# Performance work log

Measured on AMD Instinct MI355X. Metric: run time of the kernel, lower is better.

## Reference

```python
import jax, jax.numpy as jnp
import numpy as np

N = 16384      # total nodes (hits)
K = 8          # n_neighbors
NB = 8         # number of graphs in batch
IN_C = 6       # in_channels
HID = 128      # hidden_channels
NCLS = 3       # num_classes
SLOPE = 0.2    # GATv2 leaky_relu negative_slope
BIG = 1e30     # mask value for cross-graph pairs


def setup_inputs() -> dict:
    key = jax.random.key(0)
    ks = jax.random.split(key, 32)
    coord = jax.random.normal(ks[0], (N, 3), dtype=jnp.float32)
    feat = jax.random.normal(ks[1], (N, IN_C), dtype=jnp.float32)
    batch = jnp.sort(jax.random.randint(ks[2], (N,), 0, NB)).astype(jnp.int32)

    def lin_w(k, fan_in, fan_out):
        return (jax.random.normal(k, (fan_in, fan_out), dtype=jnp.float32)
                * np.float32(1.0 / np.sqrt(fan_in)))

    inp = {"coord": coord, "feat": feat, "batch": batch}
    dims = [IN_C, HID, HID]  # input dim of each of the 3 GATv2 layers
    kidx = 3
    for l, din in enumerate(dims):
        inp[f"Wl{l}"] = lin_w(ks[kidx], din, HID); kidx += 1
        inp[f"bl{l}"] = jnp.zeros((HID,), jnp.float32)
        inp[f"Wr{l}"] = lin_w(ks[kidx], din, HID); kidx += 1
        inp[f"br{l}"] = jnp.zeros((HID,), jnp.float32)
        inp[f"att{l}"] = (jax.random.normal(ks[kidx], (HID,), dtype=jnp.float32)
                          * np.float32(1.0 / np.sqrt(HID))); kidx += 1
        inp[f"bias{l}"] = jnp.zeros((HID,), jnp.float32)
    inp["Wf"] = lin_w(ks[kidx], HID, NCLS)
    inp["bf"] = jnp.zeros((NCLS,), jnp.float32)
    return inp


def knn_idx(coord, batch):
    # pairwise squared distances, masked so neighbors stay within the same graph
    d2 = jnp.sum((coord[:, None, :] - coord[None, :, :]) ** 2, axis=-1)  # [N,N]
    d2 = jnp.where(batch[:, None] == batch[None, :], d2, BIG)
    _, idx = jax.lax.top_k(-d2, K)  # [N,K] nearest (includes self at dist 0)
    return idx


def gatv2_layer(x, idx, Wl, bl, Wr, br, att, bias):
    xl = x @ Wl + bl                         # [N,H] source transform
    xr = x @ Wr + br                         # [N,H] target transform
    g = xl[idx]                              # [N,K,H] gather neighbor features
    e = jax.nn.leaky_relu(g + xr[:, None, :], SLOPE)
    logits = e @ att                         # [N,K] attention scores
    alpha = jax.nn.softmax(logits, axis=1)   # softmax over each node's K nbrs
    return jnp.einsum('nk,nkh->nh', alpha, g) + bias


def reference(coord, feat, batch,
              Wl0, bl0, Wr0, br0, att0, bias0,
              Wl1, bl1, Wr1, br1, att1, bias1,
              Wl2, bl2, Wr2, br2, att2, bias2,
              Wf, bf):
    idx = knn_idx(coord, batch)
    x = jax.nn.relu(gatv2_layer(feat, idx, Wl0, bl0, Wr0, br0, att0, bias0))
    x = jax.nn.relu(gatv2_layer(x, idx, Wl1, bl1, Wr1, br1, att1, bias1))
    x = jax.nn.relu(gatv2_layer(x, idx, Wl2, bl2, Wr2, br2, att2, bias2))
    return x @ Wf + bf
```

## Files before the change

### kernel.cpp

```cpp
#include <hip/hip_runtime.h>
#include <hip/hip_bf16.h>
#include <float.h>
#include <limits.h>

#define NNODES 16384
#define KNB 8
#define HIDC 128
#define KNN_CAP 2528

__device__ __forceinline__ float wave_sum(float x) {
  x += __int_as_float(__builtin_amdgcn_update_dpp(0, __float_as_int(x), 0xB1, 0xF, 0xF, true));
  x += __int_as_float(__builtin_amdgcn_update_dpp(0, __float_as_int(x), 0x4E, 0xF, 0xF, true));
  x += __int_as_float(__builtin_amdgcn_update_dpp(0, __float_as_int(x), 0x124, 0xF, 0xF, true));
  x += __int_as_float(__builtin_amdgcn_update_dpp(0, __float_as_int(x), 0x128, 0xF, 0xF, true));
  float r0 = __int_as_float(__builtin_amdgcn_readlane(__float_as_int(x), 0));
  float r1 = __int_as_float(__builtin_amdgcn_readlane(__float_as_int(x), 16));
  float r2 = __int_as_float(__builtin_amdgcn_readlane(__float_as_int(x), 32));
  float r3 = __int_as_float(__builtin_amdgcn_readlane(__float_as_int(x), 48));
  return (r0 + r1) + (r2 + r3);
}

__device__ __forceinline__ float wave_min_f32(float x) {
  x = fminf(x, __int_as_float(__builtin_amdgcn_update_dpp(0, __float_as_int(x), 0xB1, 0xF, 0xF, true)));
  x = fminf(x, __int_as_float(__builtin_amdgcn_update_dpp(0, __float_as_int(x), 0x4E, 0xF, 0xF, true)));
  x = fminf(x, __int_as_float(__builtin_amdgcn_update_dpp(0, __float_as_int(x), 0x124, 0xF, 0xF, true)));
  x = fminf(x, __int_as_float(__builtin_amdgcn_update_dpp(0, __float_as_int(x), 0x128, 0xF, 0xF, true)));
  float r0 = __int_as_float(__builtin_amdgcn_readlane(__float_as_int(x), 0));
  float r1 = __int_as_float(__builtin_amdgcn_readlane(__float_as_int(x), 16));
  float r2 = __int_as_float(__builtin_amdgcn_readlane(__float_as_int(x), 32));
  float r3 = __int_as_float(__builtin_amdgcn_readlane(__float_as_int(x), 48));
  return fminf(fminf(r0, r1), fminf(r2, r3));
}

__device__ __forceinline__ float dist2(float ax, float ay, float az,
                                       float bx, float by, float bz) {
  float dx = ax - bx, dy = ay - by, dz = az - bz;
  return fmaf(dz, dz, fmaf(dy, dy, dx * dx));
}

#define INS8V(_d, a0, a1, a2, a3, a4, a5, a6, a7)  \
  do {                                             \
    a7 = __builtin_amdgcn_fmed3f(_d, a6, a7);      \
    a6 = __builtin_amdgcn_fmed3f(_d, a5, a6);      \
    a5 = __builtin_amdgcn_fmed3f(_d, a4, a5);      \
    a4 = __builtin_amdgcn_fmed3f(_d, a3, a4);      \
    a3 = __builtin_amdgcn_fmed3f(_d, a2, a3);      \
    a2 = __builtin_amdgcn_fmed3f(_d, a1, a2);      \
    a1 = __builtin_amdgcn_fmed3f(_d, a0, a1);      \
    a0 = fminf(a0, _d);                            \
  } while (0)

__device__ __forceinline__ float merge_T(float l0, float l1, float l2, float l3,
                                         float l4, float l5, float l6, float l7,
                                         int lane) {
  float T = 0.f;
  #pragma unroll
  for (int r = 0; r < KNB; ++r) {
    float m = wave_min_f32(l0);
    T = m;
    unsigned long long msk = __ballot(l0 == m);
    int p = (int)__builtin_ctzll(msk);
    if (lane == p) { l0 = l1; l1 = l2; l2 = l3; l3 = l4; l4 = l5; l5 = l6; l6 = l7; l7 = FLT_MAX; }
  }
  return T;
}

__device__ void knn_global_single(const float* __restrict__ coord,
                                  float qx, float qy, float qz,
                                  int s, int e, int lane,
                                  int* __restrict__ knn_row) {
  float l0 = FLT_MAX, l1 = FLT_MAX, l2 = FLT_MAX, l3 = FLT_MAX,
        l4 = FLT_MAX, l5 = FLT_MAX, l6 = FLT_MAX, l7 = FLT_MAX;
  for (int base = s; base < e; base += 64) {
    int j = base + lane;
    bool ok = j < e;
    int jc = ok ? j : s;
    float d = dist2(coord[jc*3+0], coord[jc*3+1], coord[jc*3+2], qx, qy, qz);
    d = ok ? d : FLT_MAX;
    INS8V(d, l0, l1, l2, l3, l4, l5, l6, l7);
  }
  float T = merge_T(l0, l1, l2, l3, l4, l5, l6, l7, lane);
  unsigned long long lt = (1ull << lane) - 1ull;
  int cnt = 0;
  for (int base = s; base < e; base += 64) {
    int j = base + lane;
    bool ok = j < e;
    int jc = ok ? j : s;
    float d = dist2(coord[jc*3+0], coord[jc*3+1], coord[jc*3+2], qx, qy, qz);
    bool win = ok && (d <= T);
    unsigned long long msk = __ballot(win);
    if (msk) {
      int slot = cnt + __popcll(msk & lt);
      if (win && slot < KNB) knn_row[slot] = j;
      cnt += __popcll(msk);
    }
  }
}

__global__ __launch_bounds__(512) void knnlin_kernel(
    const float* __restrict__ coord, const int* __restrict__ batch,
    const float* __restrict__ feat,
    const float* __restrict__ Wl0, const float* __restrict__ bl0,
    const float* __restrict__ Wr0, const float* __restrict__ br0,
    int* __restrict__ knn, float* __restrict__ xl, float* __restrict__ xr) {
  __shared__ float4 tile[KNN_CAP];
  __shared__ int segs[9];
  int t = threadIdx.x;
  int lane = t & 63;
  int wid = t >> 6;
  int n0 = blockIdx.x * 16;

  if (t < 9) {
    int lo = 0, hi = NNODES;
    while (lo < hi) { int m = (lo + hi) >> 1; if (batch[m] < t) lo = m + 1; else hi = m; }
    segs[t] = lo;
  }
  __syncthreads();

  int b0 = batch[n0];
  int blast = batch[n0 + 15];
  int smin = segs[b0];
  int emax = segs[blast + 1];
  int win_end = min(emax, smin + KNN_CAP);
  int cnt_fill = win_end - smin;

  for (int i = t; i < cnt_fill; i += 512) {
    const float* cp = coord + (size_t)(smin + i) * 3;
    tile[i] = make_float4(cp[0], cp[1], cp[2], 0.f);
  }
  __syncthreads();

  int nA = n0 + wid * 2, nB = nA + 1;
  int bA = batch[nA], bB = batch[nB];
  int sA = segs[bA], eA = segs[bA + 1];
  bool fast = (bA == bB) && (eA - smin <= KNN_CAP);

  float ax = coord[nA*3+0], ay = coord[nA*3+1], az = coord[nA*3+2];
  float bx = coord[nB*3+0], by = coord[nB*3+1], bz = coord[nB*3+2];

  if (fast) {
    int lo_i = sA - smin;
    int M = eA - sA;
    int F = M >> 6, R = M & 63;

    float a0 = FLT_MAX, a1 = FLT_MAX, a2 = FLT_MAX, a3 = FLT_MAX,
          a4 = FLT_MAX, a5 = FLT_MAX, a6 = FLT_MAX, a7 = FLT_MAX;
    float b0r = FLT_MAX, b1 = FLT_MAX, b2 = FLT_MAX, b3 = FLT_MAX,
          b4 = FLT_MAX, b5 = FLT_MAX, b6 = FLT_MAX, b7 = FLT_MAX;
    const float4* tl = tile + lo_i;
    #pragma unroll 4
    for (int it = 0; it < F; ++it) {
      float4 c = tl[lane];
      tl += 64;
      float dA = dist2(c.x, c.y, c.z, ax, ay, az);
      float dB = dist2(c.x, c.y, c.z, bx, by, bz);
      INS8V(dA, a0, a1, a2, a3, a4, a5, a6, a7);
      INS8V(dB, b0r, b1, b2, b3, b4, b5, b6, b7);
    }
    if (R) {
      int i = lo_i + F * 64 + lane;
      bool ok = (F * 64 + lane) < M;
      float4 c = tile[ok ? i : lo_i];
      float dA = dist2(c.x, c.y, c.z, ax, ay, az);
      float dB = dist2(c.x, c.y, c.z, bx, by, bz);
      dA = ok ? dA : FLT_MAX;
      dB = ok ? dB : FLT_MAX;
      INS8V(dA, a0, a1, a2, a3, a4, a5, a6, a7);
      INS8V(dB, b0r, b1, b2, b3, b4, b5, b6, b7);
    }

    float TA = merge_T(a0, a1, a2, a3, a4, a5, a6, a7, lane);
    float TB = merge_T(b0r, b1, b2, b3, b4, b5, b6, b7, lane);

    unsigned long long lt = (1ull << lane) - 1ull;
    int cntA = 0, cntB = 0;
    const float4* tl2 = tile + lo_i;
    for (int it = 0; it < F; ++it) {
      float4 c = tl2[lane];
      tl2 += 64;
      float dA = dist2(c.x, c.y, c.z, ax, ay, az);
      float dB = dist2(c.x, c.y, c.z, bx, by, bz);
      int gidx = sA + it * 64 + lane;
      unsigned long long mA = __ballot(dA <= TA);
      if (mA) {
        int slot = cntA + __popcll(mA & lt);
        if ((dA <= TA) && slot < KNB) knn[nA*KNB + slot] = gidx;
        cntA += __popcll(mA);
      }
      unsigned long long mB = __ballot(dB <= TB);
      if (mB) {
        int slot = cntB + __popcll(mB & lt);
        if ((dB <= TB) && slot < KNB) knn[nB*KNB + slot] = gidx;
        cntB += __popcll(mB);
      }
    }
    if (R) {
      int li = F * 64 + lane;
      bool ok = li < M;
      float4 c = tile[ok ? (lo_i + li) : lo_i];
      float dA = dist2(c.x, c.y, c.z, ax, ay, az);
      float dB = dist2(c.x, c.y, c.z, bx, by, bz);
      int gidx = sA + li;
      bool wA = ok && (dA <= TA);
      bool wB = ok && (dB <= TB);
      unsigned long long mA = __ballot(wA);
      if (mA) {
        int slot = cntA + __popcll(mA & lt);
        if (wA && slot < KNB) knn[nA*KNB + slot] = gidx;
        cntA += __popcll(mA);
      }
      unsigned long long mB = __ballot(wB);
      if (mB) {
        int slot = cntB + __popcll(mB & lt);
        if (wB && slot < KNB) knn[nB*KNB + slot] = gidx;
        cntB += __popcll(mB);
      }
    }
  } else {
    int sB2 = segs[bB], eB2 = segs[bB + 1];
    knn_global_single(coord, ax, ay, az, sA, eA, lane, knn + (size_t)nA * KNB);
    knn_global_single(coord, bx, by, bz, sB2, eB2, lane, knn + (size_t)nB * KNB);
  }

  {
    int cg = t & 63;
    bool isR = cg >= 32;
    const float* W  = isR ? Wr0 : Wl0;
    const float* bi = isR ? br0 : bl0;
    float* dst      = isR ? xr : xl;
    int wc = (cg & 31) * 4;
    float4 w0 = *(const float4*)(W + 0 * HIDC + wc);
    float4 w1 = *(const float4*)(W + 1 * HIDC + wc);
    float4 w2 = *(const float4*)(W + 2 * HIDC + wc);
    float4 w3 = *(const float4*)(W + 3 * HIDC + wc);
    float4 w4 = *(const float4*)(W + 4 * HIDC + wc);
    float4 w5 = *(const float4*)(W + 5 * HIDC + wc);
    float4 bb = *(const float4*)(bi + wc);
    #pragma unroll
    for (int s2 = 0; s2 < 2; ++s2) {
      int node = n0 + wid * 2 + s2;
      const float* fr = feat + (size_t)node * 6;
      float f0 = fr[0], f1 = fr[1], f2 = fr[2], f3 = fr[3], f4 = fr[4], f5 = fr[5];
      float4 acc = make_float4(0.f, 0.f, 0.f, 0.f);
      acc.x = fmaf(f0, w0.x, acc.x); acc.y = fmaf(f0, w0.y, acc.y);
      acc.z = fmaf(f0, w0.z, acc.z); acc.w = fmaf(f0, w0.w, acc.w);
      acc.x = fmaf(f1, w1.x, acc.x); acc.y = fmaf(f1, w1.y, acc.y);
      acc.z = fmaf(f1, w1.z, acc.z); acc.w = fmaf(f1, w1.w, acc.w);
      acc.x = fmaf(f2, w2.x, acc.x); acc.y = fmaf(f2, w2.y, acc.y);
      acc.z = fmaf(f2, w2.z, acc.z); acc.w = fmaf(f2, w2.w, acc.w);
      acc.x = fmaf(f3, w3.x, acc.x); acc.y = fmaf(f3, w3.y, acc.y);
      acc.z = fmaf(f3, w3.z, acc.z); acc.w = fmaf(f3, w3.w, acc.w);
      acc.x = fmaf(f4, w4.x, acc.x); acc.y = fmaf(f4, w4.y, acc.y);
      acc.z = fmaf(f4, w4.z, acc.z); acc.w = fmaf(f4, w4.w, acc.w);
      acc.x = fmaf(f5, w5.x, acc.x); acc.y = fmaf(f5, w5.y, acc.y);
      acc.z = fmaf(f5, w5.z, acc.z); acc.w = fmaf(f5, w5.w, acc.w);
      float4 o;
      o.x = acc.x + bb.x; o.y = acc.y + bb.y;
      o.z = acc.z + bb.z; o.w = acc.w + bb.w;
      *(float4*)(dst + (size_t)node * HIDC + wc) = o;
    }
  }
}

template<int K>
__global__ __launch_bounds__(256) void lin2_kernel(
    const float* __restrict__ x,
    const float* __restrict__ Wl, const float* __restrict__ bl,
    const float* __restrict__ Wr, const float* __restrict__ br,
    float* __restrict__ xl, float* __restrict__ xr) {
  __shared__ float xs[32 * K];
  int t = threadIdx.x;
  int node0 = blockIdx.x * 32;
  for (int i = t; i < 32 * K; i += 256) xs[i] = x[node0 * K + i];
  __syncthreads();
  int cg = t & 63;
  int ng = t >> 6;
  int c0 = cg * 4;
  bool isR = (c0 >= HIDC);
  const float* W    = isR ? Wr : Wl;
  const float* bias = isR ? br : bl;
  float* dst        = isR ? xr : xl;
  int wc = isR ? (c0 - HIDC) : c0;

  float4 acc[8];
  #pragma unroll
  for (int nn = 0; nn < 8; ++nn) acc[nn] = make_float4(0.f, 0.f, 0.f, 0.f);

  for (int k0 = 0; k0 < K; k0 += 4) {
    float4 xv[8];
    #pragma unroll
    for (int nn = 0; nn < 8; ++nn)
      xv[nn] = *(const float4*)&xs[(ng * 8 + nn) * K + k0];
    #pragma unroll
    for (int q = 0; q < 4; ++q) {
      float4 w = *(const float4*)(W + (size_t)(k0 + q) * HIDC + wc);
      #pragma unroll
      for (int nn = 0; nn < 8; ++nn) {
        float xq = (q == 0) ? xv[nn].x : (q == 1) ? xv[nn].y : (q == 2) ? xv[nn].z : xv[nn].w;
        acc[nn].x = fmaf(xq, w.x, acc[nn].x);
        acc[nn].y = fmaf(xq, w.y, acc[nn].y);
        acc[nn].z = fmaf(xq, w.z, acc[nn].z);
        acc[nn].w = fmaf(xq, w.w, acc[nn].w);
      }
    }
  }
  float4 b4 = *(const float4*)(bias + wc);
  #pragma unroll
  for (int nn = 0; nn < 8; ++nn) {
    int node = node0 + ng * 8 + nn;
    float4 o;
    o.x = acc[nn].x + b4.x; o.y = acc[nn].y + b4.y;
    o.z = acc[nn].z + b4.z; o.w = acc[nn].w + b4.w;
    *(float4*)(dst + (size_t)node * HIDC + wc) = o;
  }
}

template<bool FINAL>
__global__ __launch_bounds__(256) void gat_attn_kernel(
    const float* __restrict__ xl, const float* __restrict__ xr,
    const int* __restrict__ knn, const float* __restrict__ att,
    const float* __restrict__ bias, float* __restrict__ xout,
    const float* __restrict__ Wf, const float* __restrict__ bf,
    float* __restrict__ out) {
  int wid = threadIdx.x >> 6;
  int lane = threadIdx.x & 63;
  int n = blockIdx.x * 4 + wid;
  int c0 = 2 * lane, c1 = 2 * lane + 1;
  float2 xr2 = *(const float2*)(xr + (size_t)n * HIDC + c0);
  float2 a2  = *(const float2*)(att + c0);
  int myj = (lane < KNB) ? knn[n * KNB + lane] : 0;
  float g0[8], g1[8], lg[8];
  #pragma unroll
  for (int k = 0; k < 8; ++k) {
    int j = __builtin_amdgcn_readlane(myj, k);
    float2 g = *(const float2*)(xl + (size_t)j * HIDC + c0);
    g0[k] = g.x; g1[k] = g.y;
    float e0 = g.x + xr2.x; e0 = (e0 > 0.f) ? e0 : 0.2f * e0;
    float e1 = g.y + xr2.y; e1 = (e1 > 0.f) ? e1 : 0.2f * e1;
    lg[k] = wave_sum(e0 * a2.x + e1 * a2.y);
  }
  float mx = lg[0];
  #pragma unroll
  for (int k = 1; k < 8; ++k) mx = fmaxf(mx, lg[k]);
  float ssum = 0.f, w[8];
  #pragma unroll
  for (int k = 0; k < 8; ++k) { w[k] = __expf(lg[k] - mx); ssum += w[k]; }
  float inv = 1.f / ssum;
  float o0 = 0.f, o1 = 0.f;
  #pragma unroll
  for (int k = 0; k < 8; ++k) { o0 += w[k] * g0[k]; o1 += w[k] * g1[k]; }
  o0 = fmaxf(fmaf(o0, inv, bias[c0]), 0.f);
  o1 = fmaxf(fmaf(o1, inv, bias[c1]), 0.f);
  if (!FINAL) {
    float2 o; o.x = o0; o.y = o1;
    *(float2*)(xout + (size_t)n * HIDC + c0) = o;
  } else {
    #pragma unroll
    for (int cls = 0; cls < 3; ++cls) {
      float p = wave_sum(o0 * Wf[c0 * 3 + cls] + o1 * Wf[c1 * 3 + cls]);
      if (lane == 0) out[n * 3 + cls] = p + bf[cls];
    }
  }
}

extern "C" void kernel_launch(void* const* d_in, const int* in_sizes, int n_in,
                              void* d_out, int out_size, void* d_ws, size_t ws_size,
                              hipStream_t stream) {
  const float* coord = (const float*)d_in[0];
  const float* feat  = (const float*)d_in[1];
  const int*   batch = (const int*)d_in[2];
  const float* Wl0 = (const float*)d_in[3];
  const float* bl0 = (const float*)d_in[4];
  const float* Wr0 = (const float*)d_in[5];
  const float* br0 = (const float*)d_in[6];
  const float* att0  = (const float*)d_in[7];
  const float* bias0 = (const float*)d_in[8];
  const float* Wl1 = (const float*)d_in[9];
  const float* bl1 = (const float*)d_in[10];
  const float* Wr1 = (const float*)d_in[11];
  const float* br1 = (const float*)d_in[12];
  const float* att1  = (const float*)d_in[13];
  const float* bias1 = (const float*)d_in[14];
  const float* Wl2 = (const float*)d_in[15];
  const float* bl2 = (const float*)d_in[16];
  const float* Wr2 = (const float*)d_in[17];
  const float* br2 = (const float*)d_in[18];
  const float* att2  = (const float*)d_in[19];
  const float* bias2 = (const float*)d_in[20];
  const float* Wf = (const float*)d_in[21];
  const float* bf = (const float*)d_in[22];
  float* out = (float*)d_out;

  char* ws = (char*)d_ws;
  int*   knn = (int*)ws;
  float* xl  = (float*)(ws + (512 << 10));
  float* xr  = xl + (size_t)NNODES * HIDC;
  float* xb0 = xr + (size_t)NNODES * HIDC;
  float* xb1 = xb0 + (size_t)NNODES * HIDC;

  knnlin_kernel<<<NNODES / 16, 512, 0, stream>>>(coord, batch, feat,
                                                 Wl0, bl0, Wr0, br0, knn, xl, xr);
  gat_attn_kernel<false><<<NNODES / 4, 256, 0, stream>>>(xl, xr, knn, att0, bias0, xb0,
                                                         nullptr, nullptr, nullptr);

  lin2_kernel<128><<<NNODES / 32, 256, 0, stream>>>(xb0, Wl1, bl1, Wr1, br1, xl, xr);
  gat_attn_kernel<false><<<NNODES / 4, 256, 0, stream>>>(xl, xr, knn, att1, bias1, xb1,
                                                         nullptr, nullptr, nullptr);

  lin2_kernel<128><<<NNODES / 32, 256, 0, stream>>>(xb1, Wl2, bl2, Wr2, br2, xl, xr);
  gat_attn_kernel<true><<<NNODES / 4, 256, 0, stream>>>(xl, xr, knn, att2, bias2, nullptr,
                                                        Wf, bf, out);
}
```

Measured before the change: 144.6 us.

## Hoist segment search to a kernel, prefetch kNN tiles, early-exit, retile lin2

A tiny kernel now computes the graph segment boundaries once, so each kNN block no longer runs its own binary search plus a barrier. The kNN scan loops software-prefetch the next tile entry from LDS, and the selection pass stops once both query nodes have found all 8 neighbours. The kNN kernel gets a minimum-occupancy launch bound. lin2 is retiled from 32 to 16 nodes per block, which doubles the grid and lowers register pressure. Risks: the occupancy hint may cap registers and cause spills, and the early exit only pays off when the winners sit early in the segment.

```diff
diff --git a/kernel.cpp b/kernel.cpp
--- a/kernel.cpp
+++ b/kernel.cpp
@@ -97,30 +97,31 @@
   }
 }
 
-__global__ __launch_bounds__(512) void knnlin_kernel(
+__global__ void seg_kernel(const int* __restrict__ batch, int* __restrict__ seg) {
+  int b = threadIdx.x;
+  if (b > 8) return;
+  int lo = 0, hi = NNODES;
+  while (lo < hi) { int m = (lo + hi) >> 1; if (batch[m] < b) lo = m + 1; else hi = m; }
+  seg[b] = lo;
+}
+
+__global__ __launch_bounds__(512, 8) void knnlin_kernel(
     const float* __restrict__ coord, const int* __restrict__ batch,
     const float* __restrict__ feat,
     const float* __restrict__ Wl0, const float* __restrict__ bl0,
     const float* __restrict__ Wr0, const float* __restrict__ br0,
+    const int* __restrict__ seg,
     int* __restrict__ knn, float* __restrict__ xl, float* __restrict__ xr) {
   __shared__ float4 tile[KNN_CAP];
-  __shared__ int segs[9];
   int t = threadIdx.x;
   int lane = t & 63;
   int wid = t >> 6;
   int n0 = blockIdx.x * 16;
 
-  if (t < 9) {
-    int lo = 0, hi = NNODES;
-    while (lo < hi) { int m = (lo + hi) >> 1; if (batch[m] < t) lo = m + 1; else hi = m; }
-    segs[t] = lo;
-  }
-  __syncthreads();
-
   int b0 = batch[n0];
   int blast = batch[n0 + 15];
-  int smin = segs[b0];
-  int emax = segs[blast + 1];
+  int smin = seg[b0];
+  int emax = seg[blast + 1];
   int win_end = min(emax, smin + KNN_CAP);
   int cnt_fill = win_end - smin;
 
@@ -132,7 +133,7 @@
 
   int nA = n0 + wid * 2, nB = nA + 1;
   int bA = batch[nA], bB = batch[nB];
-  int sA = segs[bA], eA = segs[bA + 1];
+  int sA = seg[bA], eA = seg[bA + 1];
   bool fast = (bA == bB) && (eA - smin <= KNN_CAP);
 
   float ax = coord[nA*3+0], ay = coord[nA*3+1], az = coord[nA*3+2];
@@ -147,20 +148,22 @@
           a4 = FLT_MAX, a5 = FLT_MAX, a6 = FLT_MAX, a7 = FLT_MAX;
     float b0r = FLT_MAX, b1 = FLT_MAX, b2 = FLT_MAX, b3 = FLT_MAX,
           b4 = FLT_MAX, b5 = FLT_MAX, b6 = FLT_MAX, b7 = FLT_MAX;
-    const float4* tl = tile + lo_i;
-    #pragma unroll 4
-    for (int it = 0; it < F; ++it) {
-      float4 c = tl[lane];
-      tl += 64;
-      float dA = dist2(c.x, c.y, c.z, ax, ay, az);
-      float dB = dist2(c.x, c.y, c.z, bx, by, bz);
-      INS8V(dA, a0, a1, a2, a3, a4, a5, a6, a7);
-      INS8V(dB, b0r, b1, b2, b3, b4, b5, b6, b7);
+    if (F > 0) {
+      float4 c = tile[lo_i + lane];
+      for (int it = 0; it < F; ++it) {
+        int nxt = (it + 1 < F) ? (it + 1) : it;
+        float4 cn = tile[lo_i + nxt * 64 + lane];
+        float dA = dist2(c.x, c.y, c.z, ax, ay, az);
+        float dB = dist2(c.x, c.y, c.z, bx, by, bz);
+        INS8V(dA, a0, a1, a2, a3, a4, a5, a6, a7);
+        INS8V(dB, b0r, b1, b2, b3, b4, b5, b6, b7);
+        c = cn;
+      }
     }
     if (R) {
-      int i = lo_i + F * 64 + lane;
-      bool ok = (F * 64 + lane) < M;
-      float4 c = tile[ok ? i : lo_i];
+      int li = F * 64 + lane;
+      bool ok = li < M;
+      float4 c = tile[ok ? (lo_i + li) : lo_i];
       float dA = dist2(c.x, c.y, c.z, ax, ay, az);
       float dB = dist2(c.x, c.y, c.z, bx, by, bz);
       dA = ok ? dA : FLT_MAX;
@@ -174,27 +177,31 @@
 
     unsigned long long lt = (1ull << lane) - 1ull;
     int cntA = 0, cntB = 0;
-    const float4* tl2 = tile + lo_i;
-    for (int it = 0; it < F; ++it) {
-      float4 c = tl2[lane];
-      tl2 += 64;
-      float dA = dist2(c.x, c.y, c.z, ax, ay, az);
-      float dB = dist2(c.x, c.y, c.z, bx, by, bz);
-      int gidx = sA + it * 64 + lane;
-      unsigned long long mA = __ballot(dA <= TA);
-      if (mA) {
-        int slot = cntA + __popcll(mA & lt);
-        if ((dA <= TA) && slot < KNB) knn[nA*KNB + slot] = gidx;
-        cntA += __popcll(mA);
+    if (F > 0) {
+      float4 c = tile[lo_i + lane];
+      for (int it = 0; it < F; ++it) {
+        int nxt = (it + 1 < F) ? (it + 1) : it;
+        float4 cn = tile[lo_i + nxt * 64 + lane];
+        float dA = dist2(c.x, c.y, c.z, ax, ay, az);
+        float dB = dist2(c.x, c.y, c.z, bx, by, bz);
+        int gidx = sA + it * 64 + lane;
+        unsigned long long mA = __ballot(dA <= TA);
+        if (mA) {
+          int slot = cntA + __popcll(mA & lt);
+          if ((dA <= TA) && slot < KNB) knn[nA*KNB + slot] = gidx;
+          cntA += __popcll(mA);
+        }
+        unsigned long long mB = __ballot(dB <= TB);
+        if (mB) {
+          int slot = cntB + __popcll(mB & lt);
+          if ((dB <= TB) && slot < KNB) knn[nB*KNB + slot] = gidx;
+          cntB += __popcll(mB);
+        }
+        if (cntA >= KNB && cntB >= KNB) break;
+        c = cn;
       }
-      unsigned long long mB = __ballot(dB <= TB);
-      if (mB) {
-        int slot = cntB + __popcll(mB & lt);
-        if ((dB <= TB) && slot < KNB) knn[nB*KNB + slot] = gidx;
-        cntB += __popcll(mB);
-      }
-    }
-    if (R) {
+    }
+    if (R && (cntA < KNB || cntB < KNB)) {
       int li = F * 64 + lane;
       bool ok = li < M;
       float4 c = tile[ok ? (lo_i + li) : lo_i];
@@ -217,7 +224,7 @@
       }
     }
   } else {
-    int sB2 = segs[bB], eB2 = segs[bB + 1];
+    int sB2 = seg[bB], eB2 = seg[bB + 1];
     knn_global_single(coord, ax, ay, az, sA, eA, lane, knn + (size_t)nA * KNB);
     knn_global_single(coord, bx, by, bz, sB2, eB2, lane, knn + (size_t)nB * KNB);
   }
@@ -262,16 +269,15 @@
   }
 }
 
-template<int K>
 __global__ __launch_bounds__(256) void lin2_kernel(
     const float* __restrict__ x,
     const float* __restrict__ Wl, const float* __restrict__ bl,
     const float* __restrict__ Wr, const float* __restrict__ br,
     float* __restrict__ xl, float* __restrict__ xr) {
-  __shared__ float xs[32 * K];
+  __shared__ float xs[16 * HIDC];
   int t = threadIdx.x;
-  int node0 = blockIdx.x * 32;
-  for (int i = t; i < 32 * K; i += 256) xs[i] = x[node0 * K + i];
+  int node0 = blockIdx.x * 16;
+  for (int i = t; i < 16 * HIDC; i += 256) xs[i] = x[node0 * HIDC + i];
   __syncthreads();
   int cg = t & 63;
   int ng = t >> 6;
@@ -282,20 +288,20 @@
   float* dst        = isR ? xr : xl;
   int wc = isR ? (c0 - HIDC) : c0;
 
-  float4 acc[8];
-  #pragma unroll
-  for (int nn = 0; nn < 8; ++nn) acc[nn] = make_float4(0.f, 0.f, 0.f, 0.f);
-
-  for (int k0 = 0; k0 < K; k0 += 4) {
-    float4 xv[8];
+  float4 acc[4];
+  #pragma unroll
+  for (int nn = 0; nn < 4; ++nn) acc[nn] = make_float4(0.f, 0.f, 0.f, 0.f);
+
+  for (int k0 = 0; k0 < HIDC; k0 += 4) {
+    float4 xv[4];
     #pragma unroll
-    for (int nn = 0; nn < 8; ++nn)
-      xv[nn] = *(const float4*)&xs[(ng * 8 + nn) * K + k0];
+    for (int nn = 0; nn < 4; ++nn)
+      xv[nn] = *(const float4*)&xs[(ng * 4 + nn) * HIDC + k0];
     #pragma unroll
     for (int q = 0; q < 4; ++q) {
       float4 w = *(const float4*)(W + (size_t)(k0 + q) * HIDC + wc);
       #pragma unroll
-      for (int nn = 0; nn < 8; ++nn) {
+      for (int nn = 0; nn < 4; ++nn) {
         float xq = (q == 0) ? xv[nn].x : (q == 1) ? xv[nn].y : (q == 2) ? xv[nn].z : xv[nn].w;
         acc[nn].x = fmaf(xq, w.x, acc[nn].x);
         acc[nn].y = fmaf(xq, w.y, acc[nn].y);
@@ -306,8 +312,8 @@
   }
   float4 b4 = *(const float4*)(bias + wc);
   #pragma unroll
-  for (int nn = 0; nn < 8; ++nn) {
-    int node = node0 + ng * 8 + nn;
+  for (int nn = 0; nn < 4; ++nn) {
+    int node = node0 + ng * 4 + nn;
     float4 o;
     o.x = acc[nn].x + b4.x; o.y = acc[nn].y + b4.y;
     o.z = acc[nn].z + b4.z; o.w = acc[nn].w + b4.w;
@@ -397,17 +403,19 @@
   float* xr  = xl + (size_t)NNODES * HIDC;
   float* xb0 = xr + (size_t)NNODES * HIDC;
   float* xb1 = xb0 + (size_t)NNODES * HIDC;
-
+  int*   seg = (int*)xb1;
+
+  seg_kernel<<<1, 16, 0, stream>>>(batch, seg);
   knnlin_kernel<<<NNODES / 16, 512, 0, stream>>>(coord, batch, feat,
-                                                 Wl0, bl0, Wr0, br0, knn, xl, xr);
+                                                 Wl0, bl0, Wr0, br0, seg, knn, xl, xr);
   gat_attn_kernel<false><<<NNODES / 4, 256, 0, stream>>>(xl, xr, knn, att0, bias0, xb0,
                                                          nullptr, nullptr, nullptr);
 
-  lin2_kernel<128><<<NNODES / 32, 256, 0, stream>>>(xb0, Wl1, bl1, Wr1, br1, xl, xr);
+  lin2_kernel<<<NNODES / 16, 256, 0, stream>>>(xb0, Wl1, bl1, Wr1, br1, xl, xr);
   gat_attn_kernel<false><<<NNODES / 4, 256, 0, stream>>>(xl, xr, knn, att1, bias1, xb1,
                                                          nullptr, nullptr, nullptr);
 
-  lin2_kernel<128><<<NNODES / 32, 256, 0, stream>>>(xb1, Wl2, bl2, Wr2, br2, xl, xr);
+  lin2_kernel<<<NNODES / 16, 256, 0, stream>>>(xb1, Wl2, bl2, Wr2, br2, xl, xr);
   gat_attn_kernel<true><<<NNODES / 4, 256, 0, stream>>>(xl, xr, knn, att2, bias2, nullptr,
                                                         Wf, bf, out);
 }
```

Result: no change. 142.1 us (-1.8%).
